# Kernel tuning notes

Hardware: AMD Instinct MI355X
Metric: run time of the kernel (lower is better)

## Reference

```python
import jax, jax.numpy as jnp
import numpy as np

DIM = 512
HEADS = 8
DIM_HEAD = 64
DIM_INNER = HEADS * DIM_HEAD
FRAC_GRAD = 0.5
SCALE = DIM_HEAD ** -0.5
EPS_CUMPROD = 1e-10
EPS_INV = 1e-8


def setup_inputs() -> dict:
    key = jax.random.key(0)
    ks = jax.random.split(key, 8)
    b, n = 2, 2048
    x = jax.random.normal(ks[0], (b, n, DIM), dtype=jnp.float32)
    gamma = jnp.ones((DIM,), dtype=jnp.float32)
    w_qkv = jax.random.normal(ks[1], (DIM, 3 * DIM_INNER), dtype=jnp.float32) * 0.02
    b_qkv = jnp.zeros((3 * DIM_INNER,), dtype=jnp.float32)
    # to_a: torch init is zeros weight + bias 10; use small random weight and
    # moderate bias so the decay gate is non-trivial for correctness testing
    w_a = jax.random.normal(ks[2], (DIM, DIM_INNER), dtype=jnp.float32) * 0.02
    b_a = jnp.full((DIM_INNER,), 2.0, dtype=jnp.float32)
    w_out = jax.random.normal(ks[3], (DIM_INNER, DIM), dtype=jnp.float32) * 0.02
    b_out = jnp.zeros((DIM,), dtype=jnp.float32)
    return {"x": x, "gamma": gamma, "w_qkv": w_qkv, "b_qkv": b_qkv,
            "w_a": w_a, "b_a": b_a, "w_out": w_out, "b_out": b_out}


def _rms_norm(x, gamma):
    # F.normalize(x, dim=-1) * sqrt(dim) * gamma
    nrm = jnp.linalg.norm(x, axis=-1, keepdims=True)
    return x / jnp.maximum(nrm, 1e-12) * (DIM ** 0.5) * gamma


def _safe_cumprod(t, axis):
    t = jnp.clip(t, EPS_CUMPROD, 1.0)
    return jnp.exp(jnp.cumsum(jnp.log(t), axis=axis))


def reference(x, gamma, w_qkv, b_qkv, w_a, b_a, w_out, b_out):
    b, n, _ = x.shape
    x = _rms_norm(x, gamma)

    qkv = x @ w_qkv + b_qkv  # [b, n, 3*h*d]
    qkv = qkv.reshape(b, n, 3, HEADS, DIM_HEAD).transpose(2, 0, 3, 1, 4)  # [3,b,h,n,d]
    q, k, v = qkv[0], qkv[1], qkv[2]
    q = q * SCALE

    # data-dependent relative-position decay gate
    a = (x @ w_a + b_a).reshape(b, n, HEADS, DIM_HEAD).transpose(0, 2, 1, 3)  # [b,h,n,d]
    a = a * FRAC_GRAD + jax.lax.stop_gradient(a) * (1.0 - FRAC_GRAD)
    a = jax.nn.sigmoid(a)
    a_cum = _safe_cumprod(a, axis=-2)
    a_cum_inv = 1.0 / jnp.maximum(a_cum, EPS_INV)

    q = q * a_cum
    k = k * a_cum_inv

    sim = jnp.einsum('bhid,bhjd->bhij', q, k)
    causal_mask = jnp.triu(jnp.ones((n, n), dtype=bool), k=1)
    attn = jnp.where(causal_mask, 0.0, sim)  # no softmax in decay branch

    out = jnp.einsum('bhij,bhjd->bhid', attn, v)  # [b,h,n,d]
    out = out.transpose(0, 2, 1, 3).reshape(b, n, DIM_INNER)
    return out @ w_out + b_out
```

## Files before the change

kernel.cpp:

```cpp
#include <hip/hip_runtime.h>


using s8v   = __attribute__((ext_vector_type(8))) short;
using f32x4 = __attribute__((ext_vector_type(4))) float;

__device__ __forceinline__ unsigned short f2b(float f) {
  unsigned int u = __builtin_bit_cast(unsigned int, f);
  u += 0x7FFFu + ((u >> 16) & 1u);
  return (unsigned short)(u >> 16);
}
__device__ __forceinline__ float b2f(unsigned short b) {
  unsigned int u = ((unsigned int)b) << 16;
  return __builtin_bit_cast(float, u);
}

__device__ __forceinline__ f32x4 mfma16(s8v a, s8v b, f32x4 c) {
  return __builtin_amdgcn_mfma_f32_16x16x32_bf16(a, b, c, 0, 0, 0);
}

__device__ __forceinline__ void gload16(const void* g, void* l) {
  __builtin_amdgcn_global_load_lds(
      (const __attribute__((address_space(1))) void*)g,
      (__attribute__((address_space(3))) void*)l, 16, 0, 0);
}

__global__ __launch_bounds__(256) void prep_k(const float* __restrict__ x,
                                              const float* __restrict__ gamma,
                                              short* __restrict__ xnb,
                                              const float* __restrict__ w_qkv,
                                              const float* __restrict__ w_a,
                                              const float* __restrict__ w_out,
                                              short* __restrict__ wT,
                                              short* __restrict__ woT) {
  __shared__ float t[32][33];
  int bid = blockIdx.x;
  if (bid < 1024) {
    int row  = bid * 4 + (threadIdx.x >> 6);
    int lane = threadIdx.x & 63;
    const float4* xp = reinterpret_cast<const float4*>(x + (size_t)row * 512 + lane * 8);
    float4 v0 = xp[0], v1 = xp[1];
    float ss = v0.x*v0.x + v0.y*v0.y + v0.z*v0.z + v0.w*v0.w
             + v1.x*v1.x + v1.y*v1.y + v1.z*v1.z + v1.w*v1.w;
#pragma unroll
    for (int off = 32; off > 0; off >>= 1) ss += __shfl_xor(ss, off, 64);
    float s = 22.627416997969522f / fmaxf(sqrtf(ss), 1e-12f);
    const float* g = gamma + lane * 8;
    float vals[8] = {v0.x, v0.y, v0.z, v0.w, v1.x, v1.y, v1.z, v1.w};
    s8v o;
#pragma unroll
    for (int j = 0; j < 8; ++j) o[j] = (short)f2b(vals[j] * s * g[j]);
    *reinterpret_cast<s8v*>(xnb + (size_t)row * 512 + lane * 8) = o;
  } else {
    int id = bid - 1024;
    int bx = id % 80, k0 = (id / 80) * 32;
    const float* src; short* dst; int N, n0;
    if (bx < 48)      { src = w_qkv; dst = wT;                      N = 1536; n0 = bx * 32; }
    else if (bx < 64) { src = w_a;   dst = wT + (size_t)1536 * 512; N = 512;  n0 = (bx - 48) * 32; }
    else              { src = w_out; dst = woT;                     N = 512;  n0 = (bx - 64) * 32; }
    int tx = threadIdx.x & 31, ty = threadIdx.x >> 5;
#pragma unroll
    for (int i = 0; i < 4; ++i)
      t[ty + 8 * i][tx] = src[(size_t)(k0 + ty + 8 * i) * N + n0 + tx];
    __syncthreads();
#pragma unroll
    for (int i = 0; i < 4; ++i)
      dst[(size_t)(n0 + ty + 8 * i) * 512 + k0 + tx] = (short)f2b(t[tx][ty + 8 * i]);
  }
}

template <int BM, int BN, int EPI>
__global__ __launch_bounds__(256) void gemm_bt(const short* __restrict__ A,
                                               const short* __restrict__ Bm,
                                               void* __restrict__ Cout,
                                               const float* __restrict__ bias0,
                                               const float* __restrict__ bias1,
                                               float* __restrict__ lc,
                                               float* __restrict__ csum,
                                               int M, int N, int K) {
  constexpr int ARENA_SZ = (EPI == 0) ? (128 * 133 * 4) : (BM * 128 + BN * 128);
  __shared__ __align__(16) char ARENA[ARENA_SZ];
  char* LA = ARENA;
  char* LB = ARENA + BM * 128;
  constexpr int WM = BM / 2, WN = BN / 2, FM = WM / 16, FN = WN / 16;
  const int tid = threadIdx.x, lane = tid & 63, wave = tid >> 6;
  const int wr = (wave >> 1) * WM, wc = (wave & 1) * WN;
  const int m0 = blockIdx.y * BM, n0 = blockIdx.x * BN;
  f32x4 acc[FM][FN] = {};
  for (int k0 = 0; k0 < K; k0 += 64) {
#pragma unroll
    for (int r = 0; r < BM / 32; ++r) {
      int o = r * 4096 + tid * 16;
      int row = o >> 7;
      int ce = (((o & 127) ^ ((row & 7) << 4)) >> 1);
      gload16(A + (size_t)(m0 + row) * K + k0 + ce, LA + o);
    }
#pragma unroll
    for (int r = 0; r < BN / 32; ++r) {
      int o = r * 4096 + tid * 16;
      int row = o >> 7;
      int ce = (((o & 127) ^ ((row & 7) << 4)) >> 1);
      gload16(Bm + (size_t)(n0 + row) * K + k0 + ce, LB + o);
    }
    __syncthreads();
#pragma unroll
    for (int kk = 0; kk < 2; ++kk) {
      s8v af[FM], bf[FN];
#pragma unroll
      for (int m = 0; m < FM; ++m) {
        int row = wr + m * 16 + (lane & 15);
        int ad = ((row << 7) + kk * 64 + ((lane >> 4) << 4)) ^ ((row & 7) << 4);
        af[m] = *reinterpret_cast<const s8v*>(LA + ad);
      }
#pragma unroll
      for (int n = 0; n < FN; ++n) {
        int row = wc + n * 16 + (lane & 15);
        int ad = ((row << 7) + kk * 64 + ((lane >> 4) << 4)) ^ ((row & 7) << 4);
        bf[n] = *reinterpret_cast<const s8v*>(LB + ad);
      }
#pragma unroll
      for (int m = 0; m < FM; ++m)
#pragma unroll
        for (int n = 0; n < FN; ++n)
          acc[m][n] = mfma16(af[m], bf[n], acc[m][n]);
    }
    __syncthreads();
  }
  if constexpr (EPI == 0) {
    short* qkvb = (short*)Cout;
    if (n0 < 1536) {
#pragma unroll
      for (int m = 0; m < FM; ++m)
#pragma unroll
        for (int n = 0; n < FN; ++n)
#pragma unroll
          for (int r = 0; r < 4; ++r) {
            int row = m0 + wr + m * 16 + ((lane >> 4) << 2) + r;
            int col = n0 + wc + n * 16 + (lane & 15);
            float v = acc[m][n][r] + bias0[col];
            int w = col >> 9, h = (col >> 6) & 7, d = col & 63;
            int b = row >> 11, nn = row & 2047;
            qkvb[((((size_t)(w * 2 + b)) * 8 + h) * 2048 + nn) * 64 + d] = (short)f2b(v);
          }
    } else {
      float* L = (float*)ARENA;
#pragma unroll
      for (int m = 0; m < FM; ++m)
#pragma unroll
        for (int n = 0; n < FN; ++n)
#pragma unroll
          for (int r = 0; r < 4; ++r) {
            int rloc = wr + m * 16 + ((lane >> 4) << 2) + r;
            int cloc = wc + n * 16 + (lane & 15);
            float xv = acc[m][n][r] + bias1[n0 + cloc - 1536];
            float a = 1.f / (1.f + expf(-xv));
            a = fminf(fmaxf(a, 1e-10f), 1.f);
            L[cloc * 133 + rloc] = logf(a);
          }
      __syncthreads();
      int c = tid & 127, ch = tid >> 7;
      int gc = n0 - 1536 + c;
      int h = gc >> 6, d = gc & 63;
      int b = m0 >> 11, nbase = (m0 & 2047) + ch * 64;
      int bh = b * 8 + h;
      const float* Lp = L + c * 133 + ch * 64;
      float* lp = lc + ((size_t)bh * 2048 + nbase) * 64 + d;
      float s = 0.f;
#pragma unroll 8
      for (int i = 0; i < 64; ++i) { s += Lp[i]; lp[(size_t)i * 64] = s; }
      csum[((size_t)bh * 32 + (nbase >> 6)) * 64 + d] = s;
    }
  } else {
    float* C = (float*)Cout;
#pragma unroll
    for (int m = 0; m < FM; ++m)
#pragma unroll
      for (int n = 0; n < FN; ++n)
#pragma unroll
        for (int r = 0; r < 4; ++r) {
          int row = m0 + wr + m * 16 + ((lane >> 4) << 2) + r;
          int col = n0 + wc + n * 16 + (lane & 15);
          C[(size_t)row * N + col] = acc[m][n][r] + bias0[col];
        }
  }
}

__global__ __launch_bounds__(256) void scan2_k(const short* __restrict__ qkvb,
                                               const float* __restrict__ lc,
                                               const float* __restrict__ csum,
                                               short* __restrict__ q2,
                                               short* __restrict__ k2,
                                               short* __restrict__ vT,
                                               short* __restrict__ Sbuf) {
  int chunk = blockIdx.x, bh = blockIdx.y;
  int tid = threadIdx.x, lane = tid & 63, wave = tid >> 6;
  int b = bh >> 3, h = bh & 7, d = lane;
  __shared__ short kL[64][72], vL[64][72];
  __shared__ __align__(16) char kT[8192], vTl[8192];
  float pre = 0.f;
  for (int c = 0; c < chunk; ++c) pre += csum[((size_t)bh * 32 + c) * 64 + d];
  const size_t WS = (size_t)2 * 8 * 2048 * 64;
  size_t base = (((size_t)b * 8 + h) * 2048 + chunk * 64) * 64 + d;
  size_t rowbase = ((size_t)bh * 2048 + chunk * 64) * 64 + d;
#pragma unroll 4
  for (int rr = 0; rr < 16; ++rr) {
    int r = wave * 16 + rr;
    float s = pre + lc[rowbase + r * 64];
    float g = expf(s);
    float gi = 1.f / fmaxf(g, 1e-8f);
    float qv = b2f((unsigned short)qkvb[base + r * 64]);
    float kv = b2f((unsigned short)qkvb[base + WS + r * 64]);
    short vb = qkvb[base + 2 * WS + r * 64];
    q2[rowbase + r * 64] = (short)f2b(qv * 0.125f * g);
    unsigned short kb = f2b(kv * gi);
    k2[rowbase + r * 64] = (short)kb;
    kL[r][d] = (short)kb;
    vL[r][d] = vb;
  }
  __syncthreads();
  short* vTrow = vT + ((size_t)bh * 64 + d) * 2048 + chunk * 64;
#pragma unroll
  for (int gg = 0; gg < 2; ++gg) {
    int g8 = wave + gg * 4;
    s8v pk, pv;
#pragma unroll
    for (int j = 0; j < 8; ++j) { pk[j] = kL[g8 * 8 + j][d]; pv[j] = vL[g8 * 8 + j][d]; }
    *reinterpret_cast<s8v*>(vTrow + g8 * 8) = pv;
    int ad = ((d << 7) + g8 * 16) ^ ((d & 7) << 4);
    *reinterpret_cast<s8v*>(kT  + ad) = pk;
    *reinterpret_cast<s8v*>(vTl + ad) = pv;
  }
  __syncthreads();
  f32x4 acc[4] = {};
#pragma unroll
  for (int kk = 0; kk < 2; ++kk) {
    int arow = wave * 16 + (lane & 15);
    int aad = ((arow << 7) + kk * 64 + ((lane >> 4) << 4)) ^ ((arow & 7) << 4);
    s8v av = *reinterpret_cast<const s8v*>(vTl + aad);
#pragma unroll
    for (int n = 0; n < 4; ++n) {
      int brow = n * 16 + (lane & 15);
      int bad = ((brow << 7) + kk * 64 + ((lane >> 4) << 4)) ^ ((brow & 7) << 4);
      acc[n] = mfma16(av, *reinterpret_cast<const s8v*>(kT + bad), acc[n]);
    }
  }
  short* Sp = Sbuf + ((size_t)bh * 32 + chunk) * 4096;
#pragma unroll
  for (int n = 0; n < 4; ++n)
#pragma unroll
    for (int r = 0; r < 4; ++r)
      Sp[(wave * 16 + ((lane >> 4) << 2) + r) * 64 + n * 16 + (lane & 15)] = (short)f2b(acc[n][r]);
}

__global__ __launch_bounds__(256) void sprefix_k(const short* __restrict__ Sbuf,
                                                 short* __restrict__ Spre) {
  int bh = blockIdx.x >> 4;
  int e = ((blockIdx.x & 15) << 8) + threadIdx.x;
  size_t base = (size_t)bh * 32 * 4096 + e;
  float acc = 0.f;
  for (int c = 0; c < 32; ++c) {
    Spre[base + (size_t)c * 4096] = (short)f2b(acc);
    acc += b2f((unsigned short)Sbuf[base + (size_t)c * 4096]);
  }
}

__global__ __launch_bounds__(256) void attnk_k(const short* __restrict__ q2,
                                               const short* __restrict__ k2,
                                               const short* __restrict__ vT,
                                               const short* __restrict__ Spre,
                                               short* __restrict__ aout) {
  int chunk = blockIdx.x, bh = blockIdx.y;
  int tid = threadIdx.x, lane = tid & 63, wave = tid >> 6;
  __shared__ __align__(16) char LQ[8192], LK[8192], LV[8192], LS[8192], LP[8192];
#pragma unroll
  for (int rr = 0; rr < 2; ++rr) {
    int o = rr * 4096 + tid * 16;
    int row = o >> 7;
    int ce = (((o & 127) ^ ((row & 7) << 4)) >> 1);
    gload16(q2   + ((size_t)bh * 2048 + chunk * 64 + row) * 64 + ce, LQ + o);
    gload16(k2   + ((size_t)bh * 2048 + chunk * 64 + row) * 64 + ce, LK + o);
    gload16(vT   + ((size_t)bh * 64 + row) * 2048 + chunk * 64 + ce, LV + o);
    gload16(Spre + (((size_t)bh * 32 + chunk) * 64 + row) * 64 + ce, LS + o);
  }
  __syncthreads();
  f32x4 accS[4] = {}, accO[4] = {};
#pragma unroll
  for (int kk = 0; kk < 2; ++kk) {
    int arow = wave * 16 + (lane & 15);
    int aad = ((arow << 7) + kk * 64 + ((lane >> 4) << 4)) ^ ((arow & 7) << 4);
    s8v aq = *reinterpret_cast<const s8v*>(LQ + aad);
#pragma unroll
    for (int n = 0; n < 4; ++n) {
      int brow = n * 16 + (lane & 15);
      int bad = ((brow << 7) + kk * 64 + ((lane >> 4) << 4)) ^ ((brow & 7) << 4);
      accS[n] = mfma16(aq, *reinterpret_cast<const s8v*>(LK + bad), accS[n]);
      accO[n] = mfma16(aq, *reinterpret_cast<const s8v*>(LS + bad), accO[n]);
    }
  }
#pragma unroll
  for (int n = 0; n < 4; ++n)
#pragma unroll
    for (int r = 0; r < 4; ++r) {
      int i = wave * 16 + ((lane >> 4) << 2) + r;
      int j = n * 16 + (lane & 15);
      float v = (j <= i) ? accS[n][r] : 0.f;
      int ad = ((i << 7) + (j << 1)) ^ ((i & 7) << 4);
      *reinterpret_cast<short*>(LP + ad) = (short)f2b(v);
    }
  __syncthreads();
#pragma unroll
  for (int kk = 0; kk < 2; ++kk) {
    int arow = wave * 16 + (lane & 15);
    int aad = ((arow << 7) + kk * 64 + ((lane >> 4) << 4)) ^ ((arow & 7) << 4);
    s8v ap = *reinterpret_cast<const s8v*>(LP + aad);
#pragma unroll
    for (int n = 0; n < 4; ++n) {
      int brow = n * 16 + (lane & 15);
      int bad = ((brow << 7) + kk * 64 + ((lane >> 4) << 4)) ^ ((brow & 7) << 4);
      accO[n] = mfma16(ap, *reinterpret_cast<const s8v*>(LV + bad), accO[n]);
    }
  }
  int b = bh >> 3, h = bh & 7;
#pragma unroll
  for (int n = 0; n < 4; ++n)
#pragma unroll
    for (int r = 0; r < 4; ++r) {
      int i = wave * 16 + ((lane >> 4) << 2) + r;
      int col = h * 64 + n * 16 + (lane & 15);
      size_t row = (size_t)b * 2048 + chunk * 64 + i;
      aout[row * 512 + col] = (short)f2b(accO[n][r]);
    }
}

extern "C" void kernel_launch(void* const* d_in, const int* in_sizes, int n_in,
                              void* d_out, int out_size, void* d_ws, size_t ws_size,
                              hipStream_t stream) {
  const float* x     = (const float*)d_in[0];
  const float* gamma = (const float*)d_in[1];
  const float* w_qkv = (const float*)d_in[2];
  const float* b_qkv = (const float*)d_in[3];
  const float* w_a   = (const float*)d_in[4];
  const float* b_a   = (const float*)d_in[5];
  const float* w_out = (const float*)d_in[6];
  const float* b_out = (const float*)d_in[7];
  float* out = (float*)d_out;
  char* ws = (char*)d_ws;

  const size_t MB = 1u << 20;
  short* xnb  = (short*)(ws);
  short* wT   = (short*)(ws + 4  * MB);
  short* woT  = (short*)(ws + 6  * MB);
  short* qkvb = (short*)(ws + 7  * MB);
  float* lc   = (float*)(ws + 19 * MB);
  float* csum = (float*)(ws + 35 * MB);
  short* q2   = (short*)(ws + 36 * MB);
  short* k2   = (short*)(ws + 40 * MB);
  short* vT   = (short*)(ws + 44 * MB);
  short* Sbuf = (short*)(ws + 48 * MB);
  short* Spre = (short*)(ws + 52 * MB);
  short* aout = (short*)(ws + 56 * MB);

  prep_k<<<2304, 256, 0, stream>>>(x, gamma, xnb, w_qkv, w_a, w_out, wT, woT);

  gemm_bt<128, 128, 0><<<dim3(16, 32), 256, 0, stream>>>(
      xnb, wT, qkvb, b_qkv, b_a, lc, csum, 4096, 2048, 512);

  scan2_k<<<dim3(32, 16), 256, 0, stream>>>(qkvb, lc, csum, q2, k2, vT, Sbuf);

  sprefix_k<<<256, 256, 0, stream>>>(Sbuf, Spre);
  attnk_k<<<dim3(32, 16), 256, 0, stream>>>(q2, k2, vT, Spre, aout);

  gemm_bt<64, 64, 1><<<dim3(8, 64), 256, 0, stream>>>(
      aout, woT, out, b_out, b_out, nullptr, nullptr, 4096, 512, 512);
}
```

Baseline: 68.68 us.

## Double-buffer GEMM LDS loads, swizzle blocks across XCDs, move decay scan to scan kernel

Measured after the change: 69.66 us. About the same (+1.4%).

```diff
diff --git a/kernel.cpp b/kernel.cpp
--- a/kernel.cpp
+++ b/kernel.cpp
@@ -74,34 +74,44 @@
                                                void* __restrict__ Cout,
                                                const float* __restrict__ bias0,
                                                const float* __restrict__ bias1,
-                                               float* __restrict__ lc,
+                                               float* __restrict__ araw,
                                                float* __restrict__ csum,
                                                int M, int N, int K) {
-  constexpr int ARENA_SZ = (EPI == 0) ? (128 * 133 * 4) : (BM * 128 + BN * 128);
-  __shared__ __align__(16) char ARENA[ARENA_SZ];
-  char* LA = ARENA;
-  char* LB = ARENA + BM * 128;
+  __shared__ __align__(16) char LA[2][BM * 128];
+  __shared__ __align__(16) char LB[2][BN * 128];
   constexpr int WM = BM / 2, WN = BN / 2, FM = WM / 16, FN = WN / 16;
   const int tid = threadIdx.x, lane = tid & 63, wave = tid >> 6;
   const int wr = (wave >> 1) * WM, wc = (wave & 1) * WN;
-  const int m0 = blockIdx.y * BM, n0 = blockIdx.x * BN;
-  f32x4 acc[FM][FN] = {};
-  for (int k0 = 0; k0 < K; k0 += 64) {
+  int orig = blockIdx.y * gridDim.x + blockIdx.x;
+  int xcd = orig & 7, rq = orig >> 3;
+  int bx = rq % gridDim.x;
+  int by = xcd * (gridDim.y >> 3) + rq / gridDim.x;
+  const int m0 = by * BM, n0 = bx * BN;
+  const int NS = K / 64;
+
+  auto stage = [&](int buf, int k0) {
 #pragma unroll
     for (int r = 0; r < BM / 32; ++r) {
       int o = r * 4096 + tid * 16;
       int row = o >> 7;
       int ce = (((o & 127) ^ ((row & 7) << 4)) >> 1);
-      gload16(A + (size_t)(m0 + row) * K + k0 + ce, LA + o);
+      gload16(A + (size_t)(m0 + row) * K + k0 + ce, LA[buf] + o);
     }
 #pragma unroll
     for (int r = 0; r < BN / 32; ++r) {
       int o = r * 4096 + tid * 16;
       int row = o >> 7;
       int ce = (((o & 127) ^ ((row & 7) << 4)) >> 1);
-      gload16(Bm + (size_t)(n0 + row) * K + k0 + ce, LB + o);
-    }
-    __syncthreads();
+      gload16(Bm + (size_t)(n0 + row) * K + k0 + ce, LB[buf] + o);
+    }
+  };
+
+  f32x4 acc[FM][FN] = {};
+  stage(0, 0);
+  __syncthreads();
+  int cur = 0;
+  for (int t = 0; t < NS; ++t) {
+    if (t + 1 < NS) stage(cur ^ 1, (t + 1) * 64);
 #pragma unroll
     for (int kk = 0; kk < 2; ++kk) {
       s8v af[FM], bf[FN];
@@ -109,13 +119,13 @@
       for (int m = 0; m < FM; ++m) {
         int row = wr + m * 16 + (lane & 15);
         int ad = ((row << 7) + kk * 64 + ((lane >> 4) << 4)) ^ ((row & 7) << 4);
-        af[m] = *reinterpret_cast<const s8v*>(LA + ad);
+        af[m] = *reinterpret_cast<const s8v*>(LA[cur] + ad);
       }
 #pragma unroll
       for (int n = 0; n < FN; ++n) {
         int row = wc + n * 16 + (lane & 15);
         int ad = ((row << 7) + kk * 64 + ((lane >> 4) << 4)) ^ ((row & 7) << 4);
-        bf[n] = *reinterpret_cast<const s8v*>(LB + ad);
+        bf[n] = *reinterpret_cast<const s8v*>(LB[cur] + ad);
       }
 #pragma unroll
       for (int m = 0; m < FM; ++m)
@@ -124,7 +134,9 @@
           acc[m][n] = mfma16(af[m], bf[n], acc[m][n]);
     }
     __syncthreads();
-  }
+    cur ^= 1;
+  }
+
   if constexpr (EPI == 0) {
     short* qkvb = (short*)Cout;
     if (n0 < 1536) {
@@ -142,32 +154,35 @@
             qkvb[((((size_t)(w * 2 + b)) * 8 + h) * 2048 + nn) * 64 + d] = (short)f2b(v);
           }
     } else {
-      float* L = (float*)ARENA;
+      float cs[FN] = {};
+      int b = m0 >> 11;
 #pragma unroll
       for (int m = 0; m < FM; ++m)
 #pragma unroll
         for (int n = 0; n < FN; ++n)
 #pragma unroll
           for (int r = 0; r < 4; ++r) {
-            int rloc = wr + m * 16 + ((lane >> 4) << 2) + r;
-            int cloc = wc + n * 16 + (lane & 15);
-            float xv = acc[m][n][r] + bias1[n0 + cloc - 1536];
+            int row = m0 + wr + m * 16 + ((lane >> 4) << 2) + r;
+            int gc = n0 + wc + n * 16 + (lane & 15) - 1536;
+            int h = gc >> 6, d = gc & 63, nn = row & 2047;
+            float xv = acc[m][n][r] + bias1[gc];
+            araw[((size_t)(b * 8 + h) * 2048 + nn) * 64 + d] = xv;
             float a = 1.f / (1.f + expf(-xv));
             a = fminf(fmaxf(a, 1e-10f), 1.f);
-            L[cloc * 133 + rloc] = logf(a);
+            cs[n] += logf(a);
           }
-      __syncthreads();
-      int c = tid & 127, ch = tid >> 7;
-      int gc = n0 - 1536 + c;
+#pragma unroll
+      for (int n = 0; n < FN; ++n) {
+        cs[n] += __shfl_xor(cs[n], 16, 64);
+        cs[n] += __shfl_xor(cs[n], 32, 64);
+      }
+      int nsel = lane >> 4;
+      float v = (nsel == 0) ? cs[0] : (nsel == 1) ? cs[1] : (nsel == 2) ? cs[2] : cs[3];
+      int col = wc + nsel * 16 + (lane & 15);
+      int gc = n0 + col - 1536;
       int h = gc >> 6, d = gc & 63;
-      int b = m0 >> 11, nbase = (m0 & 2047) + ch * 64;
-      int bh = b * 8 + h;
-      const float* Lp = L + c * 133 + ch * 64;
-      float* lp = lc + ((size_t)bh * 2048 + nbase) * 64 + d;
-      float s = 0.f;
-#pragma unroll 8
-      for (int i = 0; i < 64; ++i) { s += Lp[i]; lp[(size_t)i * 64] = s; }
-      csum[((size_t)bh * 32 + (nbase >> 6)) * 64 + d] = s;
+      int chunkg = ((m0 & 2047) >> 6) + (wave >> 1);
+      csum[(((size_t)(b * 8 + h)) * 32 + chunkg) * 64 + d] = v;
     }
   } else {
     float* C = (float*)Cout;
@@ -185,7 +200,7 @@
 }
 
 __global__ __launch_bounds__(256) void scan2_k(const short* __restrict__ qkvb,
-                                               const float* __restrict__ lc,
+                                               const float* __restrict__ araw,
                                                const float* __restrict__ csum,
                                                short* __restrict__ q2,
                                                short* __restrict__ k2,
@@ -193,26 +208,39 @@
                                                short* __restrict__ Sbuf) {
   int chunk = blockIdx.x, bh = blockIdx.y;
   int tid = threadIdx.x, lane = tid & 63, wave = tid >> 6;
-  int b = bh >> 3, h = bh & 7, d = lane;
+  int d = lane;
   __shared__ short kL[64][72], vL[64][72];
+  __shared__ float wsum[4][64];
   __shared__ __align__(16) char kT[8192], vTl[8192];
   float pre = 0.f;
   for (int c = 0; c < chunk; ++c) pre += csum[((size_t)bh * 32 + c) * 64 + d];
+  const float* ap = araw + ((size_t)bh * 2048 + chunk * 64 + wave * 16) * 64 + d;
+  float la[16]; float run = 0.f;
+#pragma unroll
+  for (int rr = 0; rr < 16; ++rr) {
+    float xv = ap[rr * 64];
+    float a = 1.f / (1.f + expf(-xv));
+    a = fminf(fmaxf(a, 1e-10f), 1.f);
+    run += logf(a);
+    la[rr] = run;
+  }
+  wsum[wave][d] = run;
+  __syncthreads();
+#pragma unroll
+  for (int w = 0; w < 3; ++w) if (w < wave) pre += wsum[w][d];
   const size_t WS = (size_t)2 * 8 * 2048 * 64;
-  size_t base = (((size_t)b * 8 + h) * 2048 + chunk * 64) * 64 + d;
-  size_t rowbase = ((size_t)bh * 2048 + chunk * 64) * 64 + d;
+  size_t base = ((size_t)bh * 2048 + chunk * 64 + wave * 16) * 64 + d;
 #pragma unroll 4
   for (int rr = 0; rr < 16; ++rr) {
     int r = wave * 16 + rr;
-    float s = pre + lc[rowbase + r * 64];
-    float g = expf(s);
+    float g = expf(pre + la[rr]);
     float gi = 1.f / fmaxf(g, 1e-8f);
-    float qv = b2f((unsigned short)qkvb[base + r * 64]);
-    float kv = b2f((unsigned short)qkvb[base + WS + r * 64]);
-    short vb = qkvb[base + 2 * WS + r * 64];
-    q2[rowbase + r * 64] = (short)f2b(qv * 0.125f * g);
+    float qv = b2f((unsigned short)qkvb[base + rr * 64]);
+    float kv = b2f((unsigned short)qkvb[base + WS + rr * 64]);
+    short vb = qkvb[base + 2 * WS + rr * 64];
+    q2[base + rr * 64] = (short)f2b(qv * 0.125f * g);
     unsigned short kb = f2b(kv * gi);
-    k2[rowbase + r * 64] = (short)kb;
+    k2[base + rr * 64] = (short)kb;
     kL[r][d] = (short)kb;
     vL[r][d] = vb;
   }
@@ -350,21 +378,21 @@
   short* wT   = (short*)(ws + 4  * MB);
   short* woT  = (short*)(ws + 6  * MB);
   short* qkvb = (short*)(ws + 7  * MB);
-  float* lc   = (float*)(ws + 19 * MB);
-  float* csum = (float*)(ws + 35 * MB);
-  short* q2   = (short*)(ws + 36 * MB);
-  short* k2   = (short*)(ws + 40 * MB);
-  short* vT   = (short*)(ws + 44 * MB);
-  short* Sbuf = (short*)(ws + 48 * MB);
-  short* Spre = (short*)(ws + 52 * MB);
-  short* aout = (short*)(ws + 56 * MB);
+  float* araw = (float*)(ws + 19 * MB);
+  float* csum = (float*)(ws + 27 * MB);
+  short* q2   = (short*)(ws + 28 * MB);
+  short* k2   = (short*)(ws + 32 * MB);
+  short* vT   = (short*)(ws + 36 * MB);
+  short* Sbuf = (short*)(ws + 40 * MB);
+  short* Spre = (short*)(ws + 44 * MB);
+  short* aout = (short*)(ws + 48 * MB);
 
   prep_k<<<2304, 256, 0, stream>>>(x, gamma, xnb, w_qkv, w_a, w_out, wT, woT);
 
   gemm_bt<128, 128, 0><<<dim3(16, 32), 256, 0, stream>>>(
-      xnb, wT, qkvb, b_qkv, b_a, lc, csum, 4096, 2048, 512);
-
-  scan2_k<<<dim3(32, 16), 256, 0, stream>>>(qkvb, lc, csum, q2, k2, vT, Sbuf);
+      xnb, wT, qkvb, b_qkv, b_a, araw, csum, 4096, 2048, 512);
+
+  scan2_k<<<dim3(32, 16), 256, 0, stream>>>(qkvb, araw, csum, q2, k2, vT, Sbuf);
 
   sprefix_k<<<256, 256, 0, stream>>>(Sbuf, Spre);
   attnk_k<<<dim3(32, 16), 256, 0, stream>>>(q2, k2, vT, Spre, aout);
```
